# Kernel tuning notes

Hardware: AMD Instinct MI355X
Metric: run time of the kernel (lower is better)

Reference implementation:

```python
import jax, jax.numpy as jnp
import numpy as np

TEMPERATURE = 12.5   # init temperature
SINKHORN_EPS = 0.05  # entropic regularization replacing exact cv2.EMD LP solve
SINKHORN_ITERS = 100 # fixed iteration count (jit-friendly)


def _weight_vector(A, B):
    # A: [M,C,H,W], B: [N,C,H,W] -> [M, N, H*W]
    # matches: global-avg-pool B over HW, inner product over channels per spatial node of A
    Bp = B.mean(axis=(2, 3))                      # [N, C]
    comb = jnp.einsum('mchw,nc->mnhw', A, Bp)     # [M, N, H, W]
    comb = comb.reshape(A.shape[0], B.shape[0], -1)
    return jax.nn.relu(comb) + 0.001


def _center(x):
    # norm='center': subtract channel mean (dim 1)
    return x - x.mean(axis=1, keepdims=True)


def _similarity_map(support, query):
    # metric='cosine': sim[q, w, i, j] = cos(query[q,:,i], support[w,:,j]) over channels
    s = support.reshape(support.shape[0], support.shape[1], -1)  # [W, C, Ns]
    q = query.reshape(query.shape[0], query.shape[1], -1)        # [Q, C, Nq]
    s = s / jnp.maximum(jnp.linalg.norm(s, axis=1, keepdims=True), 1e-8)
    q = q / jnp.maximum(jnp.linalg.norm(q, axis=1, keepdims=True), 1e-8)
    return jnp.einsum('qci,wcj->qwij', q, s)                     # [Q, W, Nq, Ns]


def _sinkhorn_flow(cost, a, b, eps=SINKHORN_EPS, n_iters=SINKHORN_ITERS):
    # Batched entropic OT in log-space. cost: [..., n, m]; a: [..., n]; b: [..., m].
    log_a = jnp.log(a)
    log_b = jnp.log(b)
    logK = -cost / eps

    def body(_, uv):
        u, v = uv
        u = log_a - jax.nn.logsumexp(logK + v[..., None, :], axis=-1)
        v = log_b - jax.nn.logsumexp(logK + u[..., None], axis=-2)
        return (u, v)

    u0 = jnp.zeros_like(log_a)
    v0 = jnp.zeros_like(log_b)
    u, v = jax.lax.fori_loop(0, n_iters, body, (u0, v0))
    return jnp.exp(logK + u[..., None] + v[..., None, :])  # transport plan [..., n, m]


def setup_inputs() -> dict:
    key = jax.random.key(0)
    k1, k2 = jax.random.split(key)
    support = jax.random.normal(k1, (32, 512, 8, 8), dtype=jnp.float32)
    query = jax.random.normal(k2, (256, 512, 8, 8), dtype=jnp.float32)
    return {"support": support, "query": query}


def reference(support, query):
    # weight_1: [Q, W, N] (row/query-node marginals), weight_2: [W, Q, N] (col/support-node)
    w1 = _weight_vector(query, support)
    w2 = _weight_vector(support, query)

    s = _center(support)
    q = _center(query)
    sim = _similarity_map(s, q)  # [Q, W, N, N]

    num_node = w1.shape[-1]
    # opencv path: relu (no-op, already >0) + 1e-5, rescale so each marginal sums to num_node
    a = w1 + 1e-5
    a = a * (num_node / a.sum(-1, keepdims=True))              # [Q, W, N]
    b = jnp.transpose(w2, (1, 0, 2)) + 1e-5                    # weight_2[j, i] -> [Q, W, N]
    b = b * (num_node / b.sum(-1, keepdims=True))

    flow = _sinkhorn_flow(1.0 - sim, a, b)                     # [Q, W, N, N]
    flow = jax.lax.stop_gradient(flow)  # opencv flow is a non-differentiable constant

    logits = (sim * flow).sum((-1, -2)) * (TEMPERATURE / num_node)  # [Q, W]
    return logits
```

## Files before the change

kernel.cpp:

```cpp
#include <hip/hip_runtime.h>
#include <math.h>


#define DEV static __device__ __forceinline__

typedef _Float16 half8 __attribute__((ext_vector_type(8)));
typedef float floatx4 __attribute__((ext_vector_type(4)));

DEV float fast_rcp(float x) {
#if __has_builtin(__builtin_amdgcn_rcpf)
    return __builtin_amdgcn_rcpf(x);
#else
    return 1.0f / x;
#endif
}
DEV float fexp2(float x) {
#if __has_builtin(__builtin_amdgcn_exp2f)
    return __builtin_amdgcn_exp2f(x);
#else
    return exp2f(x);
#endif
}
DEV float flog2(float x) {
#if __has_builtin(__builtin_amdgcn_logf)
    return __builtin_amdgcn_logf(x);
#else
    return log2f(x);
#endif
}

#define K_SIM2M 28.853900817779268f
#define K_M2SIM 0.034657359027997264f
#define LDPH 72

__global__ void __launch_bounds__(1024, 1)
norm_kernel(const float* __restrict__ support, const float* __restrict__ query,
            _Float16* __restrict__ Vht, _Float16* __restrict__ Uht,
            _Float16* __restrict__ Bp16, _Float16* __restrict__ Qp16,
            float* __restrict__ muA, float* __restrict__ nrmA,
            float* __restrict__ Ssc) {
    __shared__ float red1[16][64];
    __shared__ float red2[16][64];
    __shared__ float muL[64], invL[64];
    __shared__ float tile[128][65];

    int sid = blockIdx.x;
    const float* src;
    _Float16* dst;
    _Float16* poolT;
    int pidx;
    if (sid < 32) {
        src = support + (size_t)sid * 32768; dst = Vht + (size_t)sid * 32768;
        poolT = Bp16; pidx = sid;
    } else {
        src = query + (size_t)(sid - 32) * 32768; dst = Uht + (size_t)(sid - 32) * 32768;
        poolT = Qp16; pidx = sid - 32;
    }

    int node = threadIdx.x & 63;
    int cq   = threadIdx.x >> 6;

    float s1 = 0.f, s2 = 0.f;
#pragma unroll 8
    for (int j = 0; j < 32; ++j) {
        int c = cq * 32 + j;
        float x = src[c * 64 + node];
        s1 += x; s2 += x * x;
        float ps = x;
        ps += __shfl_xor(ps, 1);  ps += __shfl_xor(ps, 2);  ps += __shfl_xor(ps, 4);
        ps += __shfl_xor(ps, 8);  ps += __shfl_xor(ps, 16); ps += __shfl_xor(ps, 32);
        if (node == 0) poolT[(size_t)pidx * 512 + c] = (_Float16)(ps * (1.0f / 64.0f));
    }
    red1[cq][node] = s1;
    red2[cq][node] = s2;
    __syncthreads();
    if (threadIdx.x < 64) {
        float t1 = 0.f, t2 = 0.f;
#pragma unroll
        for (int k = 0; k < 16; ++k) { t1 += red1[k][node]; t2 += red2[k][node]; }
        float mu  = t1 * (1.0f / 512.0f);
        float ss  = t2 - 512.0f * mu * mu;
        float nrm = fmaxf(sqrtf(fmaxf(ss, 0.0f)), 1e-8f);
        muL[node]  = mu;
        invL[node] = 1.0f / nrm;
        muA[sid * 64 + node]  = mu;
        nrmA[sid * 64 + node] = nrm;
        float sS = t1;
        sS += __shfl_xor(sS, 1);  sS += __shfl_xor(sS, 2);  sS += __shfl_xor(sS, 4);
        sS += __shfl_xor(sS, 8);  sS += __shfl_xor(sS, 16); sS += __shfl_xor(sS, 32);
        if (node == 0) Ssc[sid] = sS * (1.0f / 64.0f);
    }
    __syncthreads();

    float mu = muL[node], inv = invL[node];
    for (int ch = 0; ch < 4; ++ch) {
#pragma unroll
        for (int j = 0; j < 8; ++j) {
            int cl = cq * 8 + j;
            float x = src[(ch * 128 + cl) * 64 + node];
            tile[cl][node] = (x - mu) * inv;
        }
        __syncthreads();
        {
            int g    = threadIdx.x;
            int slot = g & 63;
            int t    = (g >> 6) & 3;
            int kkl  = g >> 8;
            int nd   = t * 16 + (slot & 15);
            int c8   = (kkl << 2) | (slot >> 4);
            half8 v;
#pragma unroll
            for (int i = 0; i < 8; ++i) v[i] = (_Float16)tile[c8 * 8 + i][nd];
            *(half8*)(dst + ((size_t)ch * 1024 + g) * 8) = v;
        }
        __syncthreads();
    }
}

__global__ void __launch_bounds__(128, 2)
emd_kernel(const _Float16* __restrict__ Uht, const _Float16* __restrict__ Vht,
           const _Float16* __restrict__ Bp16, const _Float16* __restrict__ Qp16,
           const float* __restrict__ muA, const float* __restrict__ nrmA,
           const float* __restrict__ Ssc, float* __restrict__ out) {
    __shared__ __align__(16) _Float16 T[2][64 * LDPH];
    __shared__ float dAB[2][128];

    int x    = blockIdx.x & 7;
    int i    = blockIdx.x >> 3;
    int w    = i & 31;
    int wave = threadIdx.x >> 6;
    int lane = threadIdx.x & 63;
    int q    = x * 32 + (i >> 5) * 2 + wave;
    int lo16 = lane & 15;
    int hi4  = lane >> 4;
    int ig   = lane >> 3;
    int jg   = lane & 7;

    floatx4 acc[4][4];
    floatx4 accPA[4], accPB[4];
#pragma unroll
    for (int tm = 0; tm < 4; ++tm) {
#pragma unroll
        for (int tn = 0; tn < 4; ++tn)
            acc[tm][tn] = (floatx4){0.f, 0.f, 0.f, 0.f};
        accPA[tm] = (floatx4){0.f, 0.f, 0.f, 0.f};
        accPB[tm] = (floatx4){0.f, 0.f, 0.f, 0.f};
    }

    const _Float16* Abase  = Uht + (size_t)q * 32768 + lane * 8;
    const _Float16* Bbase  = Vht + (size_t)w * 32768 + lane * 8;
    const _Float16* BpBase = Bp16 + (size_t)w * 512 + hi4 * 8;
    const _Float16* QpBase = Qp16 + (size_t)q * 512 + hi4 * 8;
#pragma unroll 1
    for (int kk = 0; kk < 16; ++kk) {
        half8 bfp = *(const half8*)(BpBase + kk * 32);
        half8 afp = *(const half8*)(QpBase + kk * 32);
        half8 bf[4];
#pragma unroll
        for (int t = 0; t < 4; ++t)
            bf[t] = *(const half8*)(Bbase + (size_t)(kk * 4 + t) * 512);
#pragma unroll
        for (int tn = 0; tn < 4; ++tn)
            accPB[tn] = __builtin_amdgcn_mfma_f32_16x16x32_f16(
                afp, bf[tn], accPB[tn], 0, 0, 0);
#pragma unroll
        for (int tm = 0; tm < 4; ++tm) {
            half8 af = *(const half8*)(Abase + (size_t)(kk * 4 + tm) * 512);
#pragma unroll
            for (int tn = 0; tn < 4; ++tn)
                acc[tm][tn] = __builtin_amdgcn_mfma_f32_16x16x32_f16(
                    af, bf[tn], acc[tm][tn], 0, 0, 0);
            accPA[tm] = __builtin_amdgcn_mfma_f32_16x16x32_f16(
                af, bfp, accPA[tm], 0, 0, 0);
        }
    }

    {
        float* dA = dAB[wave];
        float* dB = dAB[wave] + 64;
        if (lo16 == 0) {
#pragma unroll
            for (int tm = 0; tm < 4; ++tm)
#pragma unroll
                for (int r = 0; r < 4; ++r)
                    dA[tm * 16 + hi4 * 4 + r] = accPA[tm][r];
        }
        if (hi4 == 0) {
#pragma unroll
            for (int tn = 0; tn < 4; ++tn)
                dB[tn * 16 + lo16] = accPB[tn][0];
        }
    }

    float lmax = -2.0f;
#pragma unroll
    for (int tm = 0; tm < 4; ++tm)
#pragma unroll
        for (int tn = 0; tn < 4; ++tn)
#pragma unroll
            for (int r = 0; r < 4; ++r) lmax = fmaxf(lmax, acc[tm][tn][r]);
    lmax = fmaxf(lmax, __shfl_xor(lmax, 1));
    lmax = fmaxf(lmax, __shfl_xor(lmax, 2));
    lmax = fmaxf(lmax, __shfl_xor(lmax, 4));
    lmax = fmaxf(lmax, __shfl_xor(lmax, 8));
    lmax = fmaxf(lmax, __shfl_xor(lmax, 16));
    lmax = fmaxf(lmax, __shfl_xor(lmax, 32));
    float s0 = lmax;

    {
        _Float16* buf = T[wave];
#pragma unroll
        for (int tm = 0; tm < 4; ++tm)
#pragma unroll
            for (int tn = 0; tn < 4; ++tn)
#pragma unroll
                for (int r = 0; r < 4; ++r) {
                    int row = tm * 16 + hi4 * 4 + r;
                    int col = tn * 16 + lo16;
                    int sp  = (col & 7) ^ (row >> 3);
                    buf[row * LDPH + (col & ~7) + sp] =
                        (_Float16)fexp2((acc[tm][tn][r] - s0) * K_SIM2M);
                }
    }
    __syncthreads();
    float Mf[8][8];
    {
        const _Float16* buf = T[wave];
#pragma unroll
        for (int t = 0; t < 8; ++t) {
            half8 h = *(const half8*)(buf + (ig * 8 + (jg ^ t)) * LDPH + jg * 8);
#pragma unroll
            for (int c = 0; c < 8; ++c) Mf[t][c] = (float)h[c];
        }
    }

    int gp = q * 32 + w;
    float a_own, b_own;
    {
        const float* dA = dAB[wave];
        const float* dB = dAB[wave] + 64;
        float Sw = Ssc[w];
        float Sq = Ssc[32 + q];
        float muq = muA[(32 + q) * 64 + lane];
        float nrq = nrmA[(32 + q) * 64 + lane];
        float va = fmaxf(fmaf(muq, Sw, nrq * dA[lane]), 0.0f) + 0.001f;
        va += 1e-5f;
        float sa = va;
        sa += __shfl_xor(sa, 1);  sa += __shfl_xor(sa, 2);  sa += __shfl_xor(sa, 4);
        sa += __shfl_xor(sa, 8);  sa += __shfl_xor(sa, 16); sa += __shfl_xor(sa, 32);
        a_own = va * (64.0f / sa);
        int nb = ((lane & 7) << 3) | (lane >> 3);
        float muw = muA[w * 64 + nb];
        float nrw = nrmA[w * 64 + nb];
        float vb = fmaxf(fmaf(muw, Sq, nrw * dB[nb]), 0.0f) + 0.001f;
        vb += 1e-5f;
        float sb = vb;
        sb += __shfl_xor(sb, 1);  sb += __shfl_xor(sb, 2);  sb += __shfl_xor(sb, 4);
        sb += __shfl_xor(sb, 8);  sb += __shfl_xor(sb, 16); sb += __shfl_xor(sb, 32);
        b_own = vb * (64.0f / sb);
    }

    float wvp[8];
#pragma unroll
    for (int s = 0; s < 8; ++s) wvp[s] = 1.0f;
    float q8[8];
    float w_prev = -1.f;

#pragma unroll 1
    for (int it = 0; it < 100; ++it) {
        float p[8];
#pragma unroll
        for (int t = 0; t < 8; ++t) {
            float s = Mf[t][0] * wvp[0];
#pragma unroll
            for (int c = 1; c < 8; ++c) s = fmaf(Mf[t][c], wvp[c], s);
            p[t] = s;
        }
        p[0] += __shfl_xor(p[4], 4); p[1] += __shfl_xor(p[5], 4);
        p[2] += __shfl_xor(p[6], 4); p[3] += __shfl_xor(p[7], 4);
        p[0] += __shfl_xor(p[2], 2); p[1] += __shfl_xor(p[3], 2);
        p[0] += __shfl_xor(p[1], 1);
        float z_own = a_own * fast_rcp(p[0]);
        q8[0] = z_own;
        q8[1] = __shfl_xor(q8[0], 1);
        q8[2] = __shfl_xor(q8[0], 2); q8[3] = __shfl_xor(q8[1], 2);
        q8[4] = __shfl_xor(q8[0], 4); q8[5] = __shfl_xor(q8[1], 4);
        q8[6] = __shfl_xor(q8[2], 4); q8[7] = __shfl_xor(q8[3], 4);
        float cp[8];
#pragma unroll
        for (int s = 0; s < 8; ++s) {
            float v = Mf[0][s] * q8[0];
#pragma unroll
            for (int t = 1; t < 8; ++t) v = fmaf(Mf[t][s], q8[t], v);
            cp[s] = v;
        }
        cp[0] += __shfl_xor(cp[4], 32); cp[1] += __shfl_xor(cp[5], 32);
        cp[2] += __shfl_xor(cp[6], 32); cp[3] += __shfl_xor(cp[7], 32);
        cp[0] += __shfl_xor(cp[2], 16); cp[1] += __shfl_xor(cp[3], 16);
        cp[0] += __shfl_xor(cp[1], 8);
        float w_own = b_own * fast_rcp(cp[0]);
        wvp[0] = w_own;
        wvp[1] = __shfl_xor(wvp[0], 8);
        wvp[2] = __shfl_xor(wvp[0], 16); wvp[3] = __shfl_xor(wvp[1], 16);
        wvp[4] = __shfl_xor(wvp[0], 32); wvp[5] = __shfl_xor(wvp[1], 32);
        wvp[6] = __shfl_xor(wvp[2], 32); wvp[7] = __shfl_xor(wvp[3], 32);
        bool same = fabsf(w_own - w_prev) <= 1e-5f * w_own;
        w_prev = w_own;
        if (__all(same)) break;
    }

    float s = 0.f;
#pragma unroll
    for (int t = 0; t < 8; ++t)
#pragma unroll
        for (int c = 0; c < 8; ++c) {
            float m    = fmaxf(Mf[t][c], 1e-30f);
            float sim  = fmaf(flog2(m), K_M2SIM, s0);
            float flow = q8[t] * m * wvp[c];
            s = fmaf(sim, flow, s);
        }
    s += __shfl_xor(s, 1);  s += __shfl_xor(s, 2);  s += __shfl_xor(s, 4);
    s += __shfl_xor(s, 8);  s += __shfl_xor(s, 16); s += __shfl_xor(s, 32);
    if (lane == 0) out[gp] = s * 0.1953125f;
}

extern "C" void kernel_launch(void* const* d_in, const int* in_sizes, int n_in,
                              void* d_out, int out_size, void* d_ws, size_t ws_size,
                              hipStream_t stream) {
    (void)in_sizes; (void)n_in; (void)out_size; (void)ws_size;
    const float* support = (const float*)d_in[0];
    const float* query   = (const float*)d_in[1];

    char* ws = (char*)d_ws;
    _Float16* Uht  = (_Float16*)ws;
    _Float16* Vht  = Uht + 8388608;
    _Float16* Bp16 = Vht + 1048576;
    _Float16* Qp16 = Bp16 + 16384;
    float* muA  = (float*)(Qp16 + 131072);
    float* nrmA = muA + 18432;
    float* Ssc  = nrmA + 18432;

    norm_kernel<<<288, 1024, 0, stream>>>(support, query, Vht, Uht, Bp16, Qp16,
                                          muA, nrmA, Ssc);
    emd_kernel<<<4096, 128, 0, stream>>>(Uht, Vht, Bp16, Qp16, muA, nrmA, Ssc,
                                         (float*)d_out);
}
```

Measured before the change: 170.2 us.

## Derive pooled weight vectors from similarity accumulators instead of separate MFMA passes

The kernel no longer computes pooled channel means in norm_kernel or runs the extra MFMAs against pooled vectors. The weight-vector dot products are instead recovered algebraically from the normalized similarity accumulators, scaled by the stored norms, and reduced with shuffles. This removes 8 MFMAs per k-step, the pooled-vector loads and the shuffle-heavy pooling in the norm kernel. Launch bounds are raised to 4 blocks per CU to increase occupancy, at the risk of register pressure and spills. Precision changes slightly because the weights now come from centered and normalized fp16 data rather than raw pooled values.

```diff
diff --git a/kernel.cpp b/kernel.cpp
--- a/kernel.cpp
+++ b/kernel.cpp
@@ -36,7 +36,6 @@
 __global__ void __launch_bounds__(1024, 1)
 norm_kernel(const float* __restrict__ support, const float* __restrict__ query,
             _Float16* __restrict__ Vht, _Float16* __restrict__ Uht,
-            _Float16* __restrict__ Bp16, _Float16* __restrict__ Qp16,
             float* __restrict__ muA, float* __restrict__ nrmA,
             float* __restrict__ Ssc) {
     __shared__ float red1[16][64];
@@ -47,14 +46,10 @@
     int sid = blockIdx.x;
     const float* src;
     _Float16* dst;
-    _Float16* poolT;
-    int pidx;
     if (sid < 32) {
         src = support + (size_t)sid * 32768; dst = Vht + (size_t)sid * 32768;
-        poolT = Bp16; pidx = sid;
     } else {
         src = query + (size_t)(sid - 32) * 32768; dst = Uht + (size_t)(sid - 32) * 32768;
-        poolT = Qp16; pidx = sid - 32;
     }
 
     int node = threadIdx.x & 63;
@@ -66,10 +61,6 @@
         int c = cq * 32 + j;
         float x = src[c * 64 + node];
         s1 += x; s2 += x * x;
-        float ps = x;
-        ps += __shfl_xor(ps, 1);  ps += __shfl_xor(ps, 2);  ps += __shfl_xor(ps, 4);
-        ps += __shfl_xor(ps, 8);  ps += __shfl_xor(ps, 16); ps += __shfl_xor(ps, 32);
-        if (node == 0) poolT[(size_t)pidx * 512 + c] = (_Float16)(ps * (1.0f / 64.0f));
     }
     red1[cq][node] = s1;
     red2[cq][node] = s2;
@@ -117,9 +108,8 @@
     }
 }
 
-__global__ void __launch_bounds__(128, 2)
+__global__ void __launch_bounds__(128, 4)
 emd_kernel(const _Float16* __restrict__ Uht, const _Float16* __restrict__ Vht,
-           const _Float16* __restrict__ Bp16, const _Float16* __restrict__ Qp16,
            const float* __restrict__ muA, const float* __restrict__ nrmA,
            const float* __restrict__ Ssc, float* __restrict__ out) {
     __shared__ __align__(16) _Float16 T[2][64 * LDPH];
@@ -137,32 +127,20 @@
     int jg   = lane & 7;
 
     floatx4 acc[4][4];
-    floatx4 accPA[4], accPB[4];
-#pragma unroll
-    for (int tm = 0; tm < 4; ++tm) {
+#pragma unroll
+    for (int tm = 0; tm < 4; ++tm)
 #pragma unroll
         for (int tn = 0; tn < 4; ++tn)
             acc[tm][tn] = (floatx4){0.f, 0.f, 0.f, 0.f};
-        accPA[tm] = (floatx4){0.f, 0.f, 0.f, 0.f};
-        accPB[tm] = (floatx4){0.f, 0.f, 0.f, 0.f};
-    }
-
-    const _Float16* Abase  = Uht + (size_t)q * 32768 + lane * 8;
-    const _Float16* Bbase  = Vht + (size_t)w * 32768 + lane * 8;
-    const _Float16* BpBase = Bp16 + (size_t)w * 512 + hi4 * 8;
-    const _Float16* QpBase = Qp16 + (size_t)q * 512 + hi4 * 8;
+
+    const _Float16* Abase = Uht + (size_t)q * 32768 + lane * 8;
+    const _Float16* Bbase = Vht + (size_t)w * 32768 + lane * 8;
 #pragma unroll 1
     for (int kk = 0; kk < 16; ++kk) {
-        half8 bfp = *(const half8*)(BpBase + kk * 32);
-        half8 afp = *(const half8*)(QpBase + kk * 32);
         half8 bf[4];
 #pragma unroll
         for (int t = 0; t < 4; ++t)
             bf[t] = *(const half8*)(Bbase + (size_t)(kk * 4 + t) * 512);
-#pragma unroll
-        for (int tn = 0; tn < 4; ++tn)
-            accPB[tn] = __builtin_amdgcn_mfma_f32_16x16x32_f16(
-                afp, bf[tn], accPB[tn], 0, 0, 0);
 #pragma unroll
         for (int tm = 0; tm < 4; ++tm) {
             half8 af = *(const half8*)(Abase + (size_t)(kk * 4 + tm) * 512);
@@ -170,12 +148,49 @@
             for (int tn = 0; tn < 4; ++tn)
                 acc[tm][tn] = __builtin_amdgcn_mfma_f32_16x16x32_f16(
                     af, bf[tn], acc[tm][tn], 0, 0, 0);
-            accPA[tm] = __builtin_amdgcn_mfma_f32_16x16x32_f16(
-                af, bfp, accPA[tm], 0, 0, 0);
         }
     }
 
     {
+        float nw[4];
+#pragma unroll
+        for (int tn = 0; tn < 4; ++tn)
+            nw[tn] = nrmA[w * 64 + tn * 16 + lo16];
+        float4 nq[4];
+#pragma unroll
+        for (int tm = 0; tm < 4; ++tm)
+            nq[tm] = *(const float4*)(nrmA + (32 + q) * 64 + tm * 16 + hi4 * 4);
+
+        float pA[4][4];
+#pragma unroll
+        for (int tm = 0; tm < 4; ++tm)
+#pragma unroll
+            for (int r = 0; r < 4; ++r) {
+                float s = acc[tm][0][r] * nw[0];
+                s = fmaf(acc[tm][1][r], nw[1], s);
+                s = fmaf(acc[tm][2][r], nw[2], s);
+                s = fmaf(acc[tm][3][r], nw[3], s);
+                s += __shfl_xor(s, 1); s += __shfl_xor(s, 2);
+                s += __shfl_xor(s, 4); s += __shfl_xor(s, 8);
+                pA[tm][r] = s;
+            }
+        float pB[4];
+#pragma unroll
+        for (int tn = 0; tn < 4; ++tn) {
+            float s = acc[0][tn][0] * nq[0].x;
+            s = fmaf(acc[0][tn][1], nq[0].y, s);
+            s = fmaf(acc[0][tn][2], nq[0].z, s);
+            s = fmaf(acc[0][tn][3], nq[0].w, s);
+#pragma unroll
+            for (int tm = 1; tm < 4; ++tm) {
+                s = fmaf(acc[tm][tn][0], nq[tm].x, s);
+                s = fmaf(acc[tm][tn][1], nq[tm].y, s);
+                s = fmaf(acc[tm][tn][2], nq[tm].z, s);
+                s = fmaf(acc[tm][tn][3], nq[tm].w, s);
+            }
+            s += __shfl_xor(s, 16); s += __shfl_xor(s, 32);
+            pB[tn] = s;
+        }
         float* dA = dAB[wave];
         float* dB = dAB[wave] + 64;
         if (lo16 == 0) {
@@ -183,12 +198,12 @@
             for (int tm = 0; tm < 4; ++tm)
 #pragma unroll
                 for (int r = 0; r < 4; ++r)
-                    dA[tm * 16 + hi4 * 4 + r] = accPA[tm][r];
+                    dA[tm * 16 + hi4 * 4 + r] = pA[tm][r] * 0.015625f;
         }
         if (hi4 == 0) {
 #pragma unroll
             for (int tn = 0; tn < 4; ++tn)
-                dB[tn * 16 + lo16] = accPB[tn][0];
+                dB[tn * 16 + lo16] = pB[tn] * 0.015625f;
         }
     }
 
@@ -334,14 +349,12 @@
     char* ws = (char*)d_ws;
     _Float16* Uht  = (_Float16*)ws;
     _Float16* Vht  = Uht + 8388608;
-    _Float16* Bp16 = Vht + 1048576;
-    _Float16* Qp16 = Bp16 + 16384;
-    float* muA  = (float*)(Qp16 + 131072);
+    float* muA  = (float*)(Vht + 1048576);
     float* nrmA = muA + 18432;
     float* Ssc  = nrmA + 18432;
 
-    norm_kernel<<<288, 1024, 0, stream>>>(support, query, Vht, Uht, Bp16, Qp16,
+    norm_kernel<<<288, 1024, 0, stream>>>(support, query, Vht, Uht,
                                           muA, nrmA, Ssc);
-    emd_kernel<<<4096, 128, 0, stream>>>(Uht, Vht, Bp16, Qp16, muA, nrmA, Ssc,
+    emd_kernel<<<4096, 128, 0, stream>>>(Uht, Vht, muA, nrmA, Ssc,
                                          (float*)d_out);
 }
```

Measured after the change: 155.5 us. 1.09x faster.
